# Performance work log

Hardware: AMD Instinct MI355X
Metric: run time of the kernel (lower is better)

## Reference

```python
import jax, jax.numpy as jnp
import numpy as np
import math

B, S, H, NH = 2, 2048, 1024, 16
DK = H // NH


def setup_inputs() -> dict:
    key = jax.random.key(0)
    k1, k2, k3 = jax.random.split(key, 3)
    scale = 1.0 / math.sqrt(H)
    return {
        "x": jax.random.normal(k1, (B, S, H), dtype=jnp.float32),
        "w_attn": jax.random.normal(k2, (H, 3 * H), dtype=jnp.float32) * scale,
        "b_attn": jnp.zeros((3 * H,), dtype=jnp.float32),
        "w_proj": jax.random.normal(k3, (H, H), dtype=jnp.float32) * scale,
        "b_proj": jnp.zeros((H,), dtype=jnp.float32),
    }


def reference(x, w_attn, b_attn, w_proj, b_proj):
    bs, seq_len, hidden = x.shape
    qkv = x @ w_attn + b_attn                       # [B,S,3H]
    q, k, v = jnp.split(qkv, 3, axis=-1)
    # [B,S,H] -> [B,NH,S,DK]
    def heads(t):
        return t.reshape(bs, seq_len, NH, DK).transpose(0, 2, 1, 3)
    q, k, v = heads(q), heads(k), heads(v)
    scores = jnp.einsum('bhqd,bhkd->bhqk', q, k) / math.sqrt(DK)  # [B,NH,S,S]
    causal = jnp.tril(jnp.ones((seq_len, seq_len), dtype=bool))
    scores = jnp.where(causal[None, None], scores, -jnp.inf)
    attn = jax.nn.softmax(scores, axis=-1)
    out = jnp.einsum('bhqk,bhkd->bhqd', attn, v)    # [B,NH,S,DK]
    out = out.transpose(0, 2, 1, 3).reshape(bs, seq_len, hidden)
    return out @ w_proj + b_proj
```

## Files before the change

### kernel.cpp

```cpp
#include <hip/hip_runtime.h>

#define BATCH 2
#define S_LEN 2048
#define NHEADS 16
#define DKV 64
#define HID 1024

typedef __attribute__((ext_vector_type(8))) short s16x8;
typedef __attribute__((ext_vector_type(4))) short s16x4;
typedef __attribute__((ext_vector_type(4))) float f32x4;

__device__ inline unsigned short f2bf(float f) {
    union { float f; unsigned int u; } v; v.f = f;
    unsigned int r = v.u + 0x7fffu + ((v.u >> 16) & 1u);
    return (unsigned short)(r >> 16);
}

__device__ inline s16x8 pack8(float4 a, float4 b) {
    s16x8 r;
    r[0] = (short)f2bf(a.x); r[1] = (short)f2bf(a.y);
    r[2] = (short)f2bf(a.z); r[3] = (short)f2bf(a.w);
    r[4] = (short)f2bf(b.x); r[5] = (short)f2bf(b.y);
    r[6] = (short)f2bf(b.z); r[7] = (short)f2bf(b.w);
    return r;
}

__device__ inline void gload_lds16(const void* g, void* l) {
    __builtin_amdgcn_global_load_lds(
        (const __attribute__((address_space(1))) void*)g,
        (__attribute__((address_space(3))) void*)l, 16, 0, 0);
}

__device__ inline unsigned int cvtpk_bf16(float lo, float hi) {
    unsigned int d;
    asm("v_cvt_pk_bf16_f32 %0, %1, %2" : "=v"(d) : "v"(lo), "v"(hi));
    return d;
}

__global__ __launch_bounds__(256)
void prep_kernel(const float* __restrict__ x, unsigned short* __restrict__ xb,
                 const float* __restrict__ w_attn, unsigned short* __restrict__ waT,
                 const float* __restrict__ w_proj, unsigned short* __restrict__ wpT) {
    __shared__ float tile[32][33];
    const int blk = blockIdx.x;
    const int tid = threadIdx.x;

    if (blk < 2048) {
        int i = blk * 256 + tid;
        const float4* p = (const float4*)(x + (size_t)i * 8);
        float4 a = p[0], b = p[1];
        *(s16x8*)(xb + (size_t)i * 8) = pack8(a, b);
        return;
    }

    const float* in;
    unsigned short* outp;
    int n0, k0, N;
    if (blk < 5120) {
        int idx = blk - 2048;
        N = 3 * HID;
        n0 = (idx % 96) * 32; k0 = (idx / 96) * 32;
        in = w_attn; outp = waT;
    } else {
        int idx = blk - 5120;
        N = HID;
        n0 = (idx % 32) * 32; k0 = (idx / 32) * 32;
        in = w_proj; outp = wpT;
    }
    const int tx = tid & 31, ty = tid >> 5;
    for (int i = ty; i < 32; i += 8)
        tile[i][tx] = in[(size_t)(k0 + i) * N + n0 + tx];
    __syncthreads();
    {
        const int n  = tid >> 3;
        const int kc = (tid & 7) * 4;
        s16x4 pk;
        #pragma unroll
        for (int j = 0; j < 4; j++) pk[j] = (short)f2bf(tile[kc + j][n]);
        *(s16x4*)&outp[(size_t)(n0 + n) * HID + k0 + kc] = pk;
    }
}

__global__ __launch_bounds__(256)
void gemm_qkv_kernel(const unsigned short* __restrict__ A, const unsigned short* __restrict__ Bt,
                     const float* __restrict__ bias, unsigned short* __restrict__ qkv,
                     unsigned short* __restrict__ vT, int M, int N, int K) {
    __shared__ __align__(16) unsigned short As[2][128 * 32];
    __shared__ __align__(16) unsigned short Bs[2][128 * 32];

    const int tid  = threadIdx.x;
    const int lane = tid & 63;
    const int wv   = tid >> 6;
    const int wr   = wv >> 1, wc = wv & 1;
    const int m0   = blockIdx.y * 128, n0 = blockIdx.x * 128;

    const int lr = lane & 15;
    const int lg = lane >> 4;
    const int lk = lg * 8;

    const int srow = lane >> 2;
    const int scol = (lane & 3) * 8;

    f32x4 acc[4][4] = {};
    int cur = 0;

    #pragma unroll
    for (int l = 0; l < 2; l++) {
        const int r0 = wv * 32 + l * 16;
        gload_lds16(A  + (size_t)(m0 + r0 + srow) * K + scol, &As[0][r0 * 32]);
        gload_lds16(Bt + (size_t)(n0 + r0 + srow) * K + scol, &Bs[0][r0 * 32]);
    }

    for (int k0 = 0; k0 < K; k0 += 32) {
        __syncthreads();

        if (k0 + 32 < K) {
            #pragma unroll
            for (int l = 0; l < 2; l++) {
                const int r0 = wv * 32 + l * 16;
                gload_lds16(A  + (size_t)(m0 + r0 + srow) * K + k0 + 32 + scol, &As[cur ^ 1][r0 * 32]);
                gload_lds16(Bt + (size_t)(n0 + r0 + srow) * K + k0 + 32 + scol, &Bs[cur ^ 1][r0 * 32]);
            }
        }

        s16x8 af[4], bfr[4];
        #pragma unroll
        for (int mi = 0; mi < 4; mi++)
            af[mi] = *(const s16x8*)&As[cur][(wr * 64 + mi * 16 + lr) * 32 + lk];
        #pragma unroll
        for (int ni = 0; ni < 4; ni++)
            bfr[ni] = *(const s16x8*)&Bs[cur][(wc * 64 + ni * 16 + lr) * 32 + lk];
        #pragma unroll
        for (int mi = 0; mi < 4; mi++)
            #pragma unroll
            for (int ni = 0; ni < 4; ni++)
                acc[mi][ni] = __builtin_amdgcn_mfma_f32_16x16x32_bf16(af[mi], bfr[ni], acc[mi][ni], 0, 0, 0);
        cur ^= 1;
    }

    const bool isV = (n0 >= 2 * HID);
    const float qsc = (n0 < HID) ? 0.18033688f : 1.0f;
    #pragma unroll
    for (int mi = 0; mi < 4; mi++) {
        #pragma unroll
        for (int ni = 0; ni < 4; ni++) {
            int col = n0 + wc * 64 + ni * 16 + lr;
            float bv = bias[col];
            int row0 = m0 + wr * 64 + mi * 16 + lg * 4;
            if (isV) {
                int d = col - 2 * HID;
                int bb = row0 >> 11;
                int s = row0 & (S_LEN - 1);
                int sl = s & 63;
                int sp = (sl & 0x23) | ((sl & 0x10) >> 2) | ((sl & 0x0C) << 1);
                int sc = (s & ~63) | sp;
                s16x4 pk;
                #pragma unroll
                for (int r = 0; r < 4; r++)
                    pk[r] = (short)f2bf(acc[mi][ni][r] + bv);
                *(s16x4*)&vT[((size_t)bb * HID + d) * S_LEN + sc] = pk;
            } else {
                #pragma unroll
                for (int r = 0; r < 4; r++)
                    qkv[(size_t)(row0 + r) * (2 * HID) + col] = f2bf((acc[mi][ni][r] + bv) * qsc);
            }
        }
    }
}

__global__ __launch_bounds__(256)
void gemm64_kernel(const unsigned short* __restrict__ A, const unsigned short* __restrict__ Bt,
                   const float* __restrict__ bias, float* __restrict__ Cout,
                   int M, int N, int K) {
    __shared__ __align__(16) unsigned short As[2][64 * 32];
    __shared__ __align__(16) unsigned short Bs[2][128 * 32];

    const int tid  = threadIdx.x;
    const int lane = tid & 63;
    const int wv   = tid >> 6;
    const int wr   = wv >> 1, wc = wv & 1;
    const int m0   = blockIdx.y * 64, n0 = blockIdx.x * 128;

    const int lr = lane & 15;
    const int lg = lane >> 4;
    const int lk = lg * 8;

    const int srow = lane >> 2;
    const int scol = (lane & 3) * 8;

    const int arow = tid >> 2;
    const int acol = (tid & 3) * 8;

    f32x4 acc[2][4] = {};
    int cur = 0;

    gload_lds16(A + (size_t)(m0 + arow) * K + acol, &As[0][(arow & ~3) * 32]);
    #pragma unroll
    for (int l = 0; l < 2; l++) {
        const int r0 = wv * 32 + l * 16;
        gload_lds16(Bt + (size_t)(n0 + r0 + srow) * K + scol, &Bs[0][r0 * 32]);
    }

    for (int k0 = 0; k0 < K; k0 += 32) {
        __syncthreads();

        if (k0 + 32 < K) {
            gload_lds16(A + (size_t)(m0 + arow) * K + k0 + 32 + acol, &As[cur ^ 1][(arow & ~3) * 32]);
            #pragma unroll
            for (int l = 0; l < 2; l++) {
                const int r0 = wv * 32 + l * 16;
                gload_lds16(Bt + (size_t)(n0 + r0 + srow) * K + k0 + 32 + scol, &Bs[cur ^ 1][r0 * 32]);
            }
        }

        s16x8 af[2], bfr[4];
        #pragma unroll
        for (int mi = 0; mi < 2; mi++)
            af[mi] = *(const s16x8*)&As[cur][(wr * 32 + mi * 16 + lr) * 32 + lk];
        #pragma unroll
        for (int ni = 0; ni < 4; ni++)
            bfr[ni] = *(const s16x8*)&Bs[cur][(wc * 64 + ni * 16 + lr) * 32 + lk];
        #pragma unroll
        for (int mi = 0; mi < 2; mi++)
            #pragma unroll
            for (int ni = 0; ni < 4; ni++)
                acc[mi][ni] = __builtin_amdgcn_mfma_f32_16x16x32_bf16(af[mi], bfr[ni], acc[mi][ni], 0, 0, 0);
        cur ^= 1;
    }

    #pragma unroll
    for (int mi = 0; mi < 2; mi++) {
        #pragma unroll
        for (int ni = 0; ni < 4; ni++) {
            int col = n0 + wc * 64 + ni * 16 + lr;
            float bv = bias[col];
            #pragma unroll
            for (int r = 0; r < 4; r++) {
                int row = m0 + wr * 32 + mi * 16 + lg * 4 + r;
                Cout[(size_t)row * N + col] = acc[mi][ni][r] + bv;
            }
        }
    }
}

template<bool DIAG>
__device__ __forceinline__ void attn_tile(
    const unsigned short* __restrict__ Kt, const unsigned short* __restrict__ Vt,
    const s16x8 qf0, const s16x8 qf1, f32x4 (&o)[4], float& lsum,
    const int lr, const int lg, const int xo0, const int xo1, const int qlim)
{
    f32x4 sfT[4] = {};
    __builtin_amdgcn_s_setprio(1);
    #pragma unroll
    for (int ni = 0; ni < 4; ni++) {
        s16x8 kb = *(const s16x8*)&Kt[(ni * 16 + lr) * 64 + xo0];
        sfT[ni] = __builtin_amdgcn_mfma_f32_16x16x32_bf16(kb, qf0, sfT[ni], 0, 0, 0);
    }
    #pragma unroll
    for (int ni = 0; ni < 4; ni++) {
        s16x8 kb = *(const s16x8*)&Kt[(ni * 16 + lr) * 64 + xo1];
        sfT[ni] = __builtin_amdgcn_mfma_f32_16x16x32_bf16(kb, qf1, sfT[ni], 0, 0, 0);
    }
    __builtin_amdgcn_s_setprio(0);

    unsigned int own[4][2];
    #pragma unroll
    for (int ni = 0; ni < 4; ni++) {
        float pv[4];
        #pragma unroll
        for (int r = 0; r < 4; r++) {
            float s = sfT[ni][r];
            if (DIAG) {
                int kl = ni * 16 + lg * 4 + r;
                if (kl > qlim) s = -INFINITY;
            }
            pv[r] = exp2f(s);
        }
        lsum += (pv[0] + pv[1]) + (pv[2] + pv[3]);
        own[ni][0] = cvtpk_bf16(pv[0], pv[1]);
        own[ni][1] = cvtpk_bf16(pv[2], pv[3]);
    }

    __builtin_amdgcn_s_setprio(1);
    #pragma unroll
    for (int kt = 0; kt < 2; kt++) {
        union { unsigned int u[4]; s16x8 v; } pa;
        pa.u[0] = own[2 * kt][0];
        pa.u[1] = own[2 * kt][1];
        pa.u[2] = own[2 * kt + 1][0];
        pa.u[3] = own[2 * kt + 1][1];
        const int xo = kt ? xo1 : xo0;
        #pragma unroll
        for (int dt = 0; dt < 4; dt++) {
            s16x8 vb = *(const s16x8*)&Vt[(dt * 16 + lr) * 64 + xo];
            o[dt] = __builtin_amdgcn_mfma_f32_16x16x32_bf16(vb, pa.v, o[dt], 0, 0, 0);
        }
    }
    __builtin_amdgcn_s_setprio(0);
}

__global__ __launch_bounds__(512)
void attn_kernel(const unsigned short* __restrict__ qkv, const unsigned short* __restrict__ vT,
                 unsigned short* __restrict__ out) {
    __shared__ __align__(16) unsigned short Ks[2][2][64 * 64];
    __shared__ __align__(16) unsigned short Vs[2][2][64 * 64];

    const int tid  = threadIdx.x;
    const int lane = tid & 63;
    const int wv   = tid >> 6;
    const int grp  = wv >> 2;
    const int w    = wv & 3;

    const int wgid = blockIdx.x;
    const int xcd  = wgid & 7;
    const int slot = wgid >> 3;
    const int pp   = slot & 15;
    const int g    = (slot >> 4) * 8 + xcd;
    const int head = g & 15;
    const int b    = g >> 4;

    const size_t rowbase = (size_t)b * S_LEN;
    const int hoff = head * DKV;

    const int lr = lane & 15;
    const int lg = lane >> 4;
    const int lk = lg * 8;

    const int krow   = lane >> 3;
    const int kchunk = ((lane & 7) ^ krow) * 8;

    const int xo0 = (lg ^ (lr & 7)) * 8;
    const int xo1 = ((4 + lg) ^ (lr & 7)) * 8;
    const int qlim = w * 16 + lr;

    float* scratch = (float*)&Ks[0][0][0];

    #pragma unroll
    for (int panel = 0; panel < 2; panel++) {
        const int qb = (panel == 0) ? pp : (31 - pp);
        const int q0 = qb * 64;
        const int niter = (qb + 2) >> 1;

        s16x8 qf0, qf1;
        {
            const unsigned short* qp = qkv + (rowbase + q0 + w * 16 + lr) * (2 * HID) + hoff;
            qf0 = *(const s16x8*)(qp + lk);
            qf1 = *(const s16x8*)(qp + 32 + lk);
        }

        f32x4 o[4] = {};
        float lsum = 0.0f;
        int cur = 0;

        __syncthreads();
        if (grp <= qb) {
            const int j0 = grp * 64;
            #pragma unroll
            for (int l = 0; l < 2; l++) {
                const int r0 = (w * 2 + l) * 8;
                gload_lds16(qkv + (rowbase + j0 + r0 + krow) * (2 * HID) + HID + hoff + kchunk,
                            &Ks[grp][0][r0 * 64]);
                gload_lds16(vT + ((size_t)b * HID + hoff + r0 + krow) * S_LEN + j0 + kchunk,
                            &Vs[grp][0][r0 * 64]);
            }
        }

        for (int it = 0; it < niter; it++) {
            const int t = 2 * it + grp;
            __syncthreads();

            if (t + 2 <= qb) {
                const int jn = (t + 2) * 64;
                #pragma unroll
                for (int l = 0; l < 2; l++) {
                    const int r0 = (w * 2 + l) * 8;
                    gload_lds16(qkv + (rowbase + jn + r0 + krow) * (2 * HID) + HID + hoff + kchunk,
                                &Ks[grp][cur ^ 1][r0 * 64]);
                    gload_lds16(vT + ((size_t)b * HID + hoff + r0 + krow) * S_LEN + jn + kchunk,
                                &Vs[grp][cur ^ 1][r0 * 64]);
                }
            }

            if (t < qb) {
                attn_tile<false>(&Ks[grp][cur][0], &Vs[grp][cur][0], qf0, qf1, o, lsum,
                                 lr, lg, xo0, xo1, qlim);
            } else if (t == qb) {
                attn_tile<true>(&Ks[grp][cur][0], &Vs[grp][cur][0], qf0, qf1, o, lsum,
                                lr, lg, xo0, xo1, qlim);
            }
            cur ^= 1;
        }

        __syncthreads();
        const int sbase = (w * 64 + lane) * 17;
        if (grp == 1) {
            #pragma unroll
            for (int dt = 0; dt < 4; dt++)
                #pragma unroll
                for (int r = 0; r < 4; r++)
                    scratch[sbase + dt * 4 + r] = o[dt][r];
            scratch[sbase + 16] = lsum;
        }
        __syncthreads();
        if (grp == 0) {
            #pragma unroll
            for (int dt = 0; dt < 4; dt++)
                #pragma unroll
                for (int r = 0; r < 4; r++)
                    o[dt][r] += scratch[sbase + dt * 4 + r];
            lsum += scratch[sbase + 16];
            lsum += __shfl_xor(lsum, 16, 64);
            lsum += __shfl_xor(lsum, 32, 64);
            float invl = 1.0f / lsum;
            int qrow = q0 + w * 16 + lr;
            #pragma unroll
            for (int dt = 0; dt < 4; dt++) {
                s16x4 pk;
                #pragma unroll
                for (int r = 0; r < 4; r++) pk[r] = (short)f2bf(o[dt][r] * invl);
                *(s16x4*)&out[(rowbase + qrow) * HID + hoff + dt * 16 + lg * 4] = pk;
            }
        }
    }
}

extern "C" void kernel_launch(void* const* d_in, const int* in_sizes, int n_in,
                              void* d_out, int out_size, void* d_ws, size_t ws_size,
                              hipStream_t stream) {
    const float* x      = (const float*)d_in[0];
    const float* w_attn = (const float*)d_in[1];
    const float* b_attn = (const float*)d_in[2];
    const float* w_proj = (const float*)d_in[3];
    const float* b_proj = (const float*)d_in[4];
    float* out = (float*)d_out;

    char* ws = (char*)d_ws;
    unsigned short* qkv      = (unsigned short*)(ws);
    unsigned short* waT      = (unsigned short*)(ws + 16777216);
    unsigned short* wpT      = (unsigned short*)(ws + 23068672);
    unsigned short* attn_out = (unsigned short*)(ws + 25165824);
    unsigned short* xb       = (unsigned short*)(ws + 33554432);
    unsigned short* vTr      = (unsigned short*)(ws + 41943040);

    const int M = BATCH * S_LEN;

    prep_kernel<<<dim3(6144), 256, 0, stream>>>(x, xb, w_attn, waT, w_proj, wpT);

    gemm_qkv_kernel<<<dim3(3 * HID / 128, M / 128), 256, 0, stream>>>(
        xb, waT, b_attn, qkv, vTr, M, 3 * HID, HID);

    attn_kernel<<<dim3(512), 512, 0, stream>>>(qkv, vTr, attn_out);

    gemm64_kernel<<<dim3(HID / 128, M / 64), 256, 0, stream>>>(
        attn_out, wpT, b_proj, out, M, HID, HID);
}
```

Baseline: 109.4 us.

## Widen attention query tile to 128 rows per block, halving grid

```diff
diff --git a/kernel.cpp b/kernel.cpp
--- a/kernel.cpp
+++ b/kernel.cpp
@@ -244,66 +244,76 @@
 }
 
 template<bool DIAG>
-__device__ __forceinline__ void attn_tile(
+__device__ __forceinline__ void attn_tile32(
     const unsigned short* __restrict__ Kt, const unsigned short* __restrict__ Vt,
-    const s16x8 qf0, const s16x8 qf1, f32x4 (&o)[4], float& lsum,
-    const int lr, const int lg, const int xo0, const int xo1, const int qlim)
+    const s16x8 qf0, const s16x8 qf1, const s16x8 qg0, const s16x8 qg1,
+    f32x4 (&oA)[4], f32x4 (&oB)[4], float& lsumA, float& lsumB,
+    const int lr, const int lg, const int xo0, const int xo1,
+    const int qlimA, const int qlimB)
 {
-    f32x4 sfT[4] = {};
+    f32x4 sA[4] = {}, sB[4] = {};
     __builtin_amdgcn_s_setprio(1);
     #pragma unroll
     for (int ni = 0; ni < 4; ni++) {
         s16x8 kb = *(const s16x8*)&Kt[(ni * 16 + lr) * 64 + xo0];
-        sfT[ni] = __builtin_amdgcn_mfma_f32_16x16x32_bf16(kb, qf0, sfT[ni], 0, 0, 0);
+        sA[ni] = __builtin_amdgcn_mfma_f32_16x16x32_bf16(kb, qf0, sA[ni], 0, 0, 0);
+        sB[ni] = __builtin_amdgcn_mfma_f32_16x16x32_bf16(kb, qg0, sB[ni], 0, 0, 0);
     }
     #pragma unroll
     for (int ni = 0; ni < 4; ni++) {
         s16x8 kb = *(const s16x8*)&Kt[(ni * 16 + lr) * 64 + xo1];
-        sfT[ni] = __builtin_amdgcn_mfma_f32_16x16x32_bf16(kb, qf1, sfT[ni], 0, 0, 0);
+        sA[ni] = __builtin_amdgcn_mfma_f32_16x16x32_bf16(kb, qf1, sA[ni], 0, 0, 0);
+        sB[ni] = __builtin_amdgcn_mfma_f32_16x16x32_bf16(kb, qg1, sB[ni], 0, 0, 0);
     }
     __builtin_amdgcn_s_setprio(0);
 
-    unsigned int own[4][2];
+    unsigned int ownA[4][2], ownB[4][2];
     #pragma unroll
     for (int ni = 0; ni < 4; ni++) {
-        float pv[4];
+        float pvA[4], pvB[4];
         #pragma unroll
         for (int r = 0; r < 4; r++) {
-            float s = sfT[ni][r];
+            float sa = sA[ni][r];
+            float sb = sB[ni][r];
             if (DIAG) {
                 int kl = ni * 16 + lg * 4 + r;
-                if (kl > qlim) s = -INFINITY;
-            }
-            pv[r] = exp2f(s);
-        }
-        lsum += (pv[0] + pv[1]) + (pv[2] + pv[3]);
-        own[ni][0] = cvtpk_bf16(pv[0], pv[1]);
-        own[ni][1] = cvtpk_bf16(pv[2], pv[3]);
+                if (kl > qlimA) sa = -INFINITY;
+                if (kl > qlimB) sb = -INFINITY;
+            }
+            pvA[r] = exp2f(sa);
+            pvB[r] = exp2f(sb);
+        }
+        lsumA += (pvA[0] + pvA[1]) + (pvA[2] + pvA[3]);
+        lsumB += (pvB[0] + pvB[1]) + (pvB[2] + pvB[3]);
+        ownA[ni][0] = cvtpk_bf16(pvA[0], pvA[1]);
+        ownA[ni][1] = cvtpk_bf16(pvA[2], pvA[3]);
+        ownB[ni][0] = cvtpk_bf16(pvB[0], pvB[1]);
+        ownB[ni][1] = cvtpk_bf16(pvB[2], pvB[3]);
     }
 
     __builtin_amdgcn_s_setprio(1);
     #pragma unroll
     for (int kt = 0; kt < 2; kt++) {
-        union { unsigned int u[4]; s16x8 v; } pa;
-        pa.u[0] = own[2 * kt][0];
-        pa.u[1] = own[2 * kt][1];
-        pa.u[2] = own[2 * kt + 1][0];
-        pa.u[3] = own[2 * kt + 1][1];
+        union { unsigned int u[4]; s16x8 v; } paA, paB;
+        paA.u[0] = ownA[2 * kt][0]; paA.u[1] = ownA[2 * kt][1];
+        paA.u[2] = ownA[2 * kt + 1][0]; paA.u[3] = ownA[2 * kt + 1][1];
+        paB.u[0] = ownB[2 * kt][0]; paB.u[1] = ownB[2 * kt][1];
+        paB.u[2] = ownB[2 * kt + 1][0]; paB.u[3] = ownB[2 * kt + 1][1];
         const int xo = kt ? xo1 : xo0;
         #pragma unroll
         for (int dt = 0; dt < 4; dt++) {
             s16x8 vb = *(const s16x8*)&Vt[(dt * 16 + lr) * 64 + xo];
-            o[dt] = __builtin_amdgcn_mfma_f32_16x16x32_bf16(vb, pa.v, o[dt], 0, 0, 0);
+            oA[dt] = __builtin_amdgcn_mfma_f32_16x16x32_bf16(vb, paA.v, oA[dt], 0, 0, 0);
+            oB[dt] = __builtin_amdgcn_mfma_f32_16x16x32_bf16(vb, paB.v, oB[dt], 0, 0, 0);
         }
     }
     __builtin_amdgcn_s_setprio(0);
 }
 
-__global__ __launch_bounds__(512)
+__global__ __launch_bounds__(512, 2)
 void attn_kernel(const unsigned short* __restrict__ qkv, const unsigned short* __restrict__ vT,
                  unsigned short* __restrict__ out) {
-    __shared__ __align__(16) unsigned short Ks[2][2][64 * 64];
-    __shared__ __align__(16) unsigned short Vs[2][2][64 * 64];
+    __shared__ __align__(16) unsigned short lds_pool[2][2][2][64 * 64];
 
     const int tid  = threadIdx.x;
     const int lane = tid & 63;
@@ -314,8 +324,8 @@
     const int wgid = blockIdx.x;
     const int xcd  = wgid & 7;
     const int slot = wgid >> 3;
-    const int pp   = slot & 15;
-    const int g    = (slot >> 4) * 8 + xcd;
+    const int pp   = slot & 7;
+    const int g    = (slot >> 3) * 8 + xcd;
     const int head = g & 15;
     const int b    = g >> 4;
 
@@ -331,37 +341,42 @@
 
     const int xo0 = (lg ^ (lr & 7)) * 8;
     const int xo1 = ((4 + lg) ^ (lr & 7)) * 8;
-    const int qlim = w * 16 + lr;
-
-    float* scratch = (float*)&Ks[0][0][0];
+    const int qlimA = w * 32 + lr - grp * 64;
+    const int qlimB = qlimA + 16;
+
+    float* scratch = (float*)&lds_pool[0][0][0][0];
 
     #pragma unroll
     for (int panel = 0; panel < 2; panel++) {
-        const int qb = (panel == 0) ? pp : (31 - pp);
-        const int q0 = qb * 64;
-        const int niter = (qb + 2) >> 1;
-
-        s16x8 qf0, qf1;
+        const int pq = (panel == 0) ? pp : (15 - pp);
+        const int q0 = pq * 128;
+        const int nt = 2 * pq + 2;
+        const int niter = pq + 1;
+
+        s16x8 qf0, qf1, qg0, qg1;
         {
-            const unsigned short* qp = qkv + (rowbase + q0 + w * 16 + lr) * (2 * HID) + hoff;
+            const unsigned short* qp = qkv + (rowbase + q0 + w * 32 + lr) * (2 * HID) + hoff;
             qf0 = *(const s16x8*)(qp + lk);
             qf1 = *(const s16x8*)(qp + 32 + lk);
-        }
-
-        f32x4 o[4] = {};
-        float lsum = 0.0f;
+            const unsigned short* qq = qp + 16 * (2 * HID);
+            qg0 = *(const s16x8*)(qq + lk);
+            qg1 = *(const s16x8*)(qq + 32 + lk);
+        }
+
+        f32x4 oA[4] = {}, oB[4] = {};
+        float lsumA = 0.0f, lsumB = 0.0f;
         int cur = 0;
 
         __syncthreads();
-        if (grp <= qb) {
+        {
             const int j0 = grp * 64;
             #pragma unroll
             for (int l = 0; l < 2; l++) {
                 const int r0 = (w * 2 + l) * 8;
                 gload_lds16(qkv + (rowbase + j0 + r0 + krow) * (2 * HID) + HID + hoff + kchunk,
-                            &Ks[grp][0][r0 * 64]);
+                            &lds_pool[grp][0][0][r0 * 64]);
                 gload_lds16(vT + ((size_t)b * HID + hoff + r0 + krow) * S_LEN + j0 + kchunk,
-                            &Vs[grp][0][r0 * 64]);
+                            &lds_pool[grp][0][1][r0 * 64]);
             }
         }
 
@@ -369,56 +384,71 @@
             const int t = 2 * it + grp;
             __syncthreads();
 
-            if (t + 2 <= qb) {
+            if (t + 2 < nt) {
                 const int jn = (t + 2) * 64;
                 #pragma unroll
                 for (int l = 0; l < 2; l++) {
                     const int r0 = (w * 2 + l) * 8;
                     gload_lds16(qkv + (rowbase + jn + r0 + krow) * (2 * HID) + HID + hoff + kchunk,
-                                &Ks[grp][cur ^ 1][r0 * 64]);
+                                &lds_pool[grp][cur ^ 1][0][r0 * 64]);
                     gload_lds16(vT + ((size_t)b * HID + hoff + r0 + krow) * S_LEN + jn + kchunk,
-                                &Vs[grp][cur ^ 1][r0 * 64]);
+                                &lds_pool[grp][cur ^ 1][1][r0 * 64]);
                 }
             }
 
-            if (t < qb) {
-                attn_tile<false>(&Ks[grp][cur][0], &Vs[grp][cur][0], qf0, qf1, o, lsum,
-                                 lr, lg, xo0, xo1, qlim);
-            } else if (t == qb) {
-                attn_tile<true>(&Ks[grp][cur][0], &Vs[grp][cur][0], qf0, qf1, o, lsum,
-                                lr, lg, xo0, xo1, qlim);
+            if (it == niter - 1) {
+                attn_tile32<true>(&lds_pool[grp][cur][0][0], &lds_pool[grp][cur][1][0],
+                                  qf0, qf1, qg0, qg1, oA, oB, lsumA, lsumB,
+                                  lr, lg, xo0, xo1, qlimA, qlimB);
+            } else {
+                attn_tile32<false>(&lds_pool[grp][cur][0][0], &lds_pool[grp][cur][1][0],
+                                   qf0, qf1, qg0, qg1, oA, oB, lsumA, lsumB,
+                                   lr, lg, xo0, xo1, qlimA, qlimB);
             }
             cur ^= 1;
         }
 
         __syncthreads();
-        const int sbase = (w * 64 + lane) * 17;
+        const int sbase = (w * 64 + lane) * 35;
         if (grp == 1) {
             #pragma unroll
             for (int dt = 0; dt < 4; dt++)
                 #pragma unroll
-                for (int r = 0; r < 4; r++)
-                    scratch[sbase + dt * 4 + r] = o[dt][r];
-            scratch[sbase + 16] = lsum;
+                for (int r = 0; r < 4; r++) {
+                    scratch[sbase + dt * 4 + r]      = oA[dt][r];
+                    scratch[sbase + 16 + dt * 4 + r] = oB[dt][r];
+                }
+            scratch[sbase + 32] = lsumA;
+            scratch[sbase + 33] = lsumB;
         }
         __syncthreads();
         if (grp == 0) {
             #pragma unroll
             for (int dt = 0; dt < 4; dt++)
                 #pragma unroll
-                for (int r = 0; r < 4; r++)
-                    o[dt][r] += scratch[sbase + dt * 4 + r];
-            lsum += scratch[sbase + 16];
-            lsum += __shfl_xor(lsum, 16, 64);
-            lsum += __shfl_xor(lsum, 32, 64);
-            float invl = 1.0f / lsum;
-            int qrow = q0 + w * 16 + lr;
+                for (int r = 0; r < 4; r++) {
+                    oA[dt][r] += scratch[sbase + dt * 4 + r];
+                    oB[dt][r] += scratch[sbase + 16 + dt * 4 + r];
+                }
+            lsumA += scratch[sbase + 32];
+            lsumB += scratch[sbase + 33];
+            lsumA += __shfl_xor(lsumA, 16, 64);
+            lsumA += __shfl_xor(lsumA, 32, 64);
+            lsumB += __shfl_xor(lsumB, 16, 64);
+            lsumB += __shfl_xor(lsumB, 32, 64);
+            float invlA = 1.0f / lsumA;
+            float invlB = 1.0f / lsumB;
+            const int qrowA = q0 + w * 32 + lr;
             #pragma unroll
             for (int dt = 0; dt < 4; dt++) {
-                s16x4 pk;
-                #pragma unroll
-                for (int r = 0; r < 4; r++) pk[r] = (short)f2bf(o[dt][r] * invl);
-                *(s16x4*)&out[(rowbase + qrow) * HID + hoff + dt * 16 + lg * 4] = pk;
+                s16x4 pkA, pkB;
+                #pragma unroll
+                for (int r = 0; r < 4; r++) {
+                    pkA[r] = (short)f2bf(oA[dt][r] * invlA);
+                    pkB[r] = (short)f2bf(oB[dt][r] * invlB);
+                }
+                *(s16x4*)&out[(rowbase + qrowA) * HID + hoff + dt * 16 + lg * 4]      = pkA;
+                *(s16x4*)&out[(rowbase + qrowA + 16) * HID + hoff + dt * 16 + lg * 4] = pkB;
             }
         }
     }
@@ -449,7 +479,7 @@
     gemm_qkv_kernel<<<dim3(3 * HID / 128, M / 128), 256, 0, stream>>>(
         xb, waT, b_attn, qkv, vTr, M, 3 * HID, HID);
 
-    attn_kernel<<<dim3(512), 512, 0, stream>>>(qkv, vTr, attn_out);
+    attn_kernel<<<dim3(256), 512, 0, stream>>>(qkv, vTr, attn_out);
 
     gemm64_kernel<<<dim3(HID / 128, M / 64), 256, 0, stream>>>(
         attn_out, wpT, b_proj, out, M, HID, HID);
```

New measurement: 105.3 us (median of 2 runs). 3.7% less time.
